# Kernel optimization log

Measured on AMD Instinct MI355X. Metric: run time of the kernel, lower is better.

The kernel has to match this reference:

```python
import jax, jax.numpy as jnp
import numpy as np

D_MODEL = 1024
NUM_HEADS = 16
HEAD_DIM = D_MODEL // NUM_HEADS
B, S = 4, 2048


def setup_inputs() -> dict:
    key = jax.random.key(0)
    ks = jax.random.split(key, 12)
    s = 1.0 / np.sqrt(D_MODEL)
    return {
        "inputs_q": jax.random.normal(ks[0], (B, S, D_MODEL), jnp.float32),
        "inputs_k": jax.random.normal(ks[1], (B, S, D_MODEL), jnp.float32),
        "inputs_v": jax.random.normal(ks[2], (B, S, D_MODEL), jnp.float32),
        "Wq": jax.random.normal(ks[3], (D_MODEL, D_MODEL), jnp.float32) * s,
        "bq": jax.random.normal(ks[4], (D_MODEL,), jnp.float32) * 0.01,
        "Wk": jax.random.normal(ks[5], (D_MODEL, D_MODEL), jnp.float32) * s,
        "bk": jax.random.normal(ks[6], (D_MODEL,), jnp.float32) * 0.01,
        "Wv": jax.random.normal(ks[7], (D_MODEL, D_MODEL), jnp.float32) * s,
        "bv": jax.random.normal(ks[8], (D_MODEL,), jnp.float32) * 0.01,
        "Wo": jax.random.normal(ks[9], (D_MODEL, D_MODEL), jnp.float32) * s,
        "bo": jax.random.normal(ks[10], (D_MODEL,), jnp.float32) * 0.01,
    }


def reference(inputs_q, inputs_k, inputs_v, Wq, bq, Wk, bk, Wv, bv, Wo, bo):
    b, s, _ = inputs_q.shape
    # linear projections
    q = inputs_q @ Wq + bq  # [b, s, d_model]
    k = inputs_k @ Wk + bk
    v = inputs_v @ Wv + bv
    # split heads: bsd -> bhsd
    q = q.reshape(b, s, NUM_HEADS, HEAD_DIM).transpose(0, 2, 1, 3)
    k = k.reshape(b, s, NUM_HEADS, HEAD_DIM).transpose(0, 2, 1, 3)
    v = v.reshape(b, s, NUM_HEADS, HEAD_DIM).transpose(0, 2, 1, 3)
    scale = 1.0 / jnp.sqrt(jnp.asarray(HEAD_DIM, q.dtype))
    scores = jnp.einsum('bhqd,bhkd->bhqk', q, k) * scale  # [b,h,s,s]
    # causal mask: position q attends to k <= q
    causal = jnp.tril(jnp.ones((s, s), dtype=bool))
    scores = jnp.where(causal[None, None], scores, jnp.asarray(-jnp.inf, scores.dtype))
    attn = jax.nn.softmax(scores, axis=-1)
    ctx = jnp.einsum('bhqk,bhkd->bhqd', attn, v)  # [b,h,s,hd]
    ctx = ctx.transpose(0, 2, 1, 3).reshape(b, s, D_MODEL)
    return ctx @ Wo + bo
```

## Files before the change

kernel.cpp:

```cpp
#include <hip/hip_runtime.h>
#include <math.h>
#include <type_traits>

typedef __bf16 bf16;
typedef __attribute__((ext_vector_type(8))) __bf16 bf16x8;
typedef __attribute__((ext_vector_type(4))) float f32x4;

#define SEQ 2048
#define DM 1024
#define NH 16
#define HD 64
#define BATCH 4

#define NEG_BIG (-1e30f)
#define SCALE_L2E 0.18033688011f

__device__ inline bf16x8 cvt_f32x8(const float* p) {
  f32x4 x0 = *(const f32x4*)p;
  f32x4 x1 = *(const f32x4*)(p + 4);
  bf16x8 r;
  r[0] = (bf16)x0[0]; r[1] = (bf16)x0[1]; r[2] = (bf16)x0[2]; r[3] = (bf16)x0[3];
  r[4] = (bf16)x1[0]; r[5] = (bf16)x1[1]; r[6] = (bf16)x1[2]; r[7] = (bf16)x1[3];
  return r;
}

__device__ inline void async_copy16(const bf16* g, bf16* l) {
  __builtin_amdgcn_global_load_lds(
      (const __attribute__((address_space(1))) unsigned int*)g,
      (__attribute__((address_space(3))) unsigned int*)l, 16, 0, 0);
}

__global__ __launch_bounds__(256) void cvt_kernel(const float* __restrict__ src,
                                                  bf16* __restrict__ dst) {
  size_t i = ((size_t)blockIdx.x * 256 + threadIdx.x) * 8;
  *(bf16x8*)(dst + i) = cvt_f32x8(src + i);
}

__global__ __launch_bounds__(256) void transpose_w_kernel(
    const float* __restrict__ Wq, const float* __restrict__ Wk,
    const float* __restrict__ Wv, const float* __restrict__ Wo,
    bf16* __restrict__ Tq, bf16* __restrict__ Tk,
    bf16* __restrict__ Tv, bf16* __restrict__ To) {
  __shared__ bf16 tile[64 * 66];
  int z = blockIdx.z;
  const float* src = (z == 0) ? Wq : (z == 1) ? Wk : (z == 2) ? Wv : Wo;
  bf16* dst = (z == 0) ? Tq : (z == 1) ? Tk : (z == 2) ? Tv : To;
  int n0 = blockIdx.x * 64, k0 = blockIdx.y * 64;
  int t = threadIdx.x;
  int c = t & 63, rr = t >> 6;
#pragma unroll
  for (int i = 0; i < 16; i++) {
    int k = i * 4 + rr;
    tile[k * 66 + c] = (bf16)src[(size_t)(k0 + k) * DM + n0 + c];
  }
  __syncthreads();
#pragma unroll
  for (int i = 0; i < 16; i++) {
    int n = i * 4 + rr;
    dst[(size_t)(n0 + n) * DM + k0 + c] = tile[c * 66 + n];
  }
}

__global__ __launch_bounds__(256) void transpose_v_kernel(
    const bf16* __restrict__ Vc, bf16* __restrict__ Vt) {
  __shared__ bf16 tile[64 * 66];
  int s0 = blockIdx.x * 64;
  int bh = blockIdx.y;
  int t = threadIdx.x;
  int c = t & 63, rr = t >> 6;
  const bf16* src = Vc + (size_t)bh * SEQ * HD;
  bf16* dst = Vt + (size_t)bh * HD * SEQ;
#pragma unroll
  for (int i = 0; i < 16; i++) {
    int s = i * 4 + rr;
    tile[s * 66 + c] = src[(size_t)(s0 + s) * HD + c];
  }
  __syncthreads();
#pragma unroll
  for (int i = 0; i < 16; i++) {
    int d = i * 4 + rr;
    dst[(size_t)d * SEQ + s0 + c] = tile[c * 66 + d];
  }
}

template <typename CT, int MODE>
__global__ __launch_bounds__(256) void gemm_bias_kernel(
    const bf16* __restrict__ A, const bf16* __restrict__ Bt,
    const float* __restrict__ bias, CT* __restrict__ C) {
  __shared__ bf16 As[128 * 32];
  __shared__ bf16 Bs[128 * 32];
  int m0 = blockIdx.x * 128, n0 = blockIdx.y * 128;
  int t = threadIdx.x;
  int wave = t >> 6, lane = t & 63, lr = lane & 15, lq = lane >> 4;
  int wm = (wave & 1) * 64, wn = (wave >> 1) * 64;

  f32x4 acc[4][4];
#pragma unroll
  for (int i = 0; i < 4; i++)
#pragma unroll
    for (int j = 0; j < 4; j++) acc[i][j] = (f32x4){0.f, 0.f, 0.f, 0.f};

  int srow = wave * 32 + (lane >> 2);
  int skc = lane & 3;
  const bf16* gA0 = A + (size_t)(m0 + srow) * DM + skc * 8;
  const bf16* gA1 = gA0 + (size_t)16 * DM;
  const bf16* gB0 = Bt + (size_t)(n0 + srow) * DM + skc * 8;
  const bf16* gB1 = gB0 + (size_t)16 * DM;
  bf16* lA0 = &As[(wave * 128) * 8];
  bf16* lA1 = &As[(wave * 128 + 64) * 8];
  bf16* lB0 = &Bs[(wave * 128) * 8];
  bf16* lB1 = &Bs[(wave * 128 + 64) * 8];

  for (int k0 = 0; k0 < DM; k0 += 32) {
    async_copy16(gA0, lA0);
    async_copy16(gA1, lA1);
    async_copy16(gB0, lB0);
    async_copy16(gB1, lB1);
    gA0 += 32; gA1 += 32; gB0 += 32; gB1 += 32;
    __syncthreads();

    bf16x8 af[4], bfr[4];
#pragma unroll
    for (int i = 0; i < 4; i++)
      af[i] = *(const bf16x8*)&As[(wm + i * 16 + lr) * 32 + lq * 8];
#pragma unroll
    for (int j = 0; j < 4; j++)
      bfr[j] = *(const bf16x8*)&Bs[(wn + j * 16 + lr) * 32 + lq * 8];
#pragma unroll
    for (int i = 0; i < 4; i++)
#pragma unroll
      for (int j = 0; j < 4; j++)
        acc[i][j] = __builtin_amdgcn_mfma_f32_16x16x32_bf16(af[i], bfr[j],
                                                            acc[i][j], 0, 0, 0);
    __syncthreads();
  }

#pragma unroll
  for (int j = 0; j < 4; j++) {
    int col = n0 + wn + j * 16 + lr;
    float bv = bias[col];
#pragma unroll
    for (int i = 0; i < 4; i++) {
      int row0 = m0 + wm + i * 16 + lq * 4;
#pragma unroll
      for (int r = 0; r < 4; r++) {
        int row = row0 + r;
        float v = acc[i][j][r] + bv;
        if constexpr (MODE == 0) {
          C[(size_t)row * DM + col] = (CT)v;
        } else {
          int b = row >> 11, s = row & 2047, h = col >> 6, d = col & 63;
          C[((size_t)(b * NH + h) * SEQ + s) * HD + d] = (CT)v;
        }
      }
    }
  }
}

__global__ __launch_bounds__(256, 2) void attention_kernel(
    const bf16* __restrict__ Qc, const bf16* __restrict__ Kc,
    const bf16* __restrict__ Vt, bf16* __restrict__ ctx) {
  int h = blockIdx.y, b = blockIdx.z;
  int t = threadIdx.x, wave = t >> 6, lane = t & 63, lr = lane & 15,
      lq = lane >> 4;

  int a = blockIdx.x * 2;
  int w4 = (wave + blockIdx.x) & 3;
  int tq = (w4 == 0) ? a : (w4 == 1) ? (63 - a) : (w4 == 2) ? (a + 1) : (62 - a);
  int q0 = tq * 32;

  const bf16* Qb = Qc + (size_t)(b * NH + h) * SEQ * HD;
  const bf16* Kb = Kc + (size_t)(b * NH + h) * SEQ * HD;
  const bf16* Vb = Vt + (size_t)(b * NH + h) * HD * SEQ;
  bf16* Cb = ctx + (size_t)b * SEQ * DM + h * HD;

  bf16x8 qf[2][2];
#pragma unroll
  for (int qi = 0; qi < 2; qi++)
#pragma unroll
    for (int ks = 0; ks < 2; ks++)
      qf[qi][ks] = *(const bf16x8*)&Qb[(size_t)(q0 + qi * 16 + lr) * HD +
                                       ks * 32 + lq * 8];

  f32x4 o[2][4];
  float m_st[2], l_st[2];
#pragma unroll
  for (int mi = 0; mi < 2; mi++) {
#pragma unroll
    for (int dj = 0; dj < 4; dj++) o[mi][dj] = (f32x4){0.f, 0.f, 0.f, 0.f};
    m_st[mi] = NEG_BIG;
    l_st[mi] = 0.f;
  }

  int kv_end = q0 + 32;
#pragma unroll 1
  for (int kv0 = 0; kv0 < kv_end; kv0 += 64) {
    bf16x8 kf[4][2];
#pragma unroll
    for (int kvt = 0; kvt < 4; kvt++)
#pragma unroll
      for (int ks = 0; ks < 2; ks++)
        kf[kvt][ks] = *(const bf16x8*)&Kb[(size_t)(kv0 + kvt * 16 + lr) * HD +
                                          ks * 32 + lq * 8];
    bf16x8 vf[4][2];
#pragma unroll
    for (int dj = 0; dj < 4; dj++)
#pragma unroll
      for (int ks2 = 0; ks2 < 2; ks2++)
        vf[dj][ks2] = *(const bf16x8*)&Vb[(size_t)(dj * 16 + lr) * SEQ + kv0 +
                                          ks2 * 32 + lq * 8];

    f32x4 s[4][2];
#pragma unroll
    for (int kvt = 0; kvt < 4; kvt++)
#pragma unroll
      for (int qi = 0; qi < 2; qi++) {
        f32x4 acc = (f32x4){0.f, 0.f, 0.f, 0.f};
        acc = __builtin_amdgcn_mfma_f32_16x16x32_bf16(kf[kvt][0], qf[qi][0],
                                                      acc, 0, 0, 0);
        acc = __builtin_amdgcn_mfma_f32_16x16x32_bf16(kf[kvt][1], qf[qi][1],
                                                      acc, 0, 0, 0);
        s[kvt][qi] = acc;
      }

    if (kv0 + 63 > q0) {
#pragma unroll
      for (int kvt = 0; kvt < 4; kvt++)
#pragma unroll
        for (int qi = 0; qi < 2; qi++)
#pragma unroll
          for (int r = 0; r < 4; r++) {
            int kv_g = kv0 + kvt * 16 + lq * 4 + r;
            int q_g = q0 + qi * 16 + lr;
            float v = s[kvt][qi][r] * SCALE_L2E;
            s[kvt][qi][r] = (kv_g > q_g) ? NEG_BIG : v;
          }
    } else {
#pragma unroll
      for (int kvt = 0; kvt < 4; kvt++)
#pragma unroll
        for (int qi = 0; qi < 2; qi++)
#pragma unroll
          for (int r = 0; r < 4; r++) s[kvt][qi][r] *= SCALE_L2E;
    }

    float alpha[2];
#pragma unroll
    for (int qi = 0; qi < 2; qi++) {
      float mx = s[0][qi][0];
#pragma unroll
      for (int kvt = 0; kvt < 4; kvt++)
#pragma unroll
        for (int r = 0; r < 4; r++) mx = fmaxf(mx, s[kvt][qi][r]);
      mx = fmaxf(mx, __shfl_xor(mx, 16));
      mx = fmaxf(mx, __shfl_xor(mx, 32));
      float mnew = fmaxf(m_st[qi], mx);
      alpha[qi] = exp2f(m_st[qi] - mnew);
      m_st[qi] = mnew;
      float rs = 0.f;
#pragma unroll
      for (int kvt = 0; kvt < 4; kvt++)
#pragma unroll
        for (int r = 0; r < 4; r++) {
          float pv = exp2f(s[kvt][qi][r] - mnew);
          s[kvt][qi][r] = pv;
          rs += pv;
        }
      rs += __shfl_xor(rs, 16);
      rs += __shfl_xor(rs, 32);
      l_st[qi] = l_st[qi] * alpha[qi] + rs;
    }

    float aT[2][4];
#pragma unroll
    for (int mi = 0; mi < 2; mi++)
#pragma unroll
      for (int r = 0; r < 4; r++) aT[mi][r] = __shfl(alpha[mi], lq * 4 + r);
#pragma unroll
    for (int mi = 0; mi < 2; mi++)
#pragma unroll
      for (int dj = 0; dj < 4; dj++)
#pragma unroll
        for (int r = 0; r < 4; r++) o[mi][dj][r] *= aT[mi][r];

    int src_base = (lq & 1) * 32 + lr;
    bool hi = (lq >> 1) != 0;
#pragma unroll
    for (int ks2 = 0; ks2 < 2; ks2++) {
      unsigned int pk0[2][2], pk1[2][2];
#pragma unroll
      for (int mi = 0; mi < 2; mi++)
#pragma unroll
        for (int w = 0; w < 2; w++) {
          unsigned int r0, r1;
          asm("v_cvt_pk_bf16_f32 %0, %1, %2"
              : "=v"(r0)
              : "v"(s[2 * ks2][mi][2 * w]), "v"(s[2 * ks2][mi][2 * w + 1]));
          asm("v_cvt_pk_bf16_f32 %0, %1, %2"
              : "=v"(r1)
              : "v"(s[2 * ks2 + 1][mi][2 * w]),
                "v"(s[2 * ks2 + 1][mi][2 * w + 1]));
          pk0[mi][w] = r0;
          pk1[mi][w] = r1;
        }
      bf16x8 pf[2];
#pragma unroll
      for (int mi = 0; mi < 2; mi++) {
#pragma unroll
        for (int w = 0; w < 4; w++) {
          int src = src_base + (w >> 1) * 16;
          unsigned int a0 = (unsigned int)__shfl((int)pk0[mi][w & 1], src);
          unsigned int a1 = (unsigned int)__shfl((int)pk1[mi][w & 1], src);
          ((unsigned int*)&pf[mi])[w] = hi ? a1 : a0;
        }
      }
#pragma unroll
      for (int dj = 0; dj < 4; dj++) {
        o[0][dj] = __builtin_amdgcn_mfma_f32_16x16x32_bf16(pf[0], vf[dj][ks2],
                                                           o[0][dj], 0, 0, 0);
        o[1][dj] = __builtin_amdgcn_mfma_f32_16x16x32_bf16(pf[1], vf[dj][ks2],
                                                           o[1][dj], 0, 0, 0);
      }
    }
  }

  float lT[2][4];
#pragma unroll
  for (int mi = 0; mi < 2; mi++)
#pragma unroll
    for (int r = 0; r < 4; r++)
      lT[mi][r] = 1.f / __shfl(l_st[mi], lq * 4 + r);
#pragma unroll
  for (int mi = 0; mi < 2; mi++)
#pragma unroll
    for (int r = 0; r < 4; r++) {
      int row = q0 + mi * 16 + lq * 4 + r;
#pragma unroll
      for (int dj = 0; dj < 4; dj++)
        Cb[(size_t)row * DM + dj * 16 + lr] = (bf16)(o[mi][dj][r] * lT[mi][r]);
    }
}

extern "C" void kernel_launch(void* const* d_in, const int* in_sizes, int n_in,
                              void* d_out, int out_size, void* d_ws,
                              size_t ws_size, hipStream_t stream) {
  const float* iq = (const float*)d_in[0];
  const float* ik = (const float*)d_in[1];
  const float* iv = (const float*)d_in[2];
  const float* Wq = (const float*)d_in[3];
  const float* bq = (const float*)d_in[4];
  const float* Wk = (const float*)d_in[5];
  const float* bk = (const float*)d_in[6];
  const float* Wv = (const float*)d_in[7];
  const float* bv = (const float*)d_in[8];
  const float* Wo = (const float*)d_in[9];
  const float* bo = (const float*)d_in[10];

  char* ws = (char*)d_ws;
  const size_t MB = 1024 * 1024;
  bf16* Tq = (bf16*)(ws + 0 * MB);
  bf16* Tk = (bf16*)(ws + 2 * MB);
  bf16* Tv = (bf16*)(ws + 4 * MB);
  bf16* To = (bf16*)(ws + 6 * MB);
  bf16* Qc = (bf16*)(ws + 8 * MB);
  bf16* Kc = (bf16*)(ws + 24 * MB);
  bf16* Vc = (bf16*)(ws + 40 * MB);
  bf16* X = (bf16*)d_out;
  bf16* Vtp = (bf16*)d_out;
  bf16* Cx = Vc;

  transpose_w_kernel<<<dim3(16, 16, 4), 256, 0, stream>>>(Wq, Wk, Wv, Wo, Tq,
                                                          Tk, Tv, To);
  cvt_kernel<<<dim3(4096), 256, 0, stream>>>(iq, X);
  gemm_bias_kernel<bf16, 1><<<dim3(64, 8), 256, 0, stream>>>(X, Tq, bq, Qc);
  cvt_kernel<<<dim3(4096), 256, 0, stream>>>(ik, X);
  gemm_bias_kernel<bf16, 1><<<dim3(64, 8), 256, 0, stream>>>(X, Tk, bk, Kc);
  cvt_kernel<<<dim3(4096), 256, 0, stream>>>(iv, X);
  gemm_bias_kernel<bf16, 1><<<dim3(64, 8), 256, 0, stream>>>(X, Tv, bv, Vc);
  transpose_v_kernel<<<dim3(32, 64), 256, 0, stream>>>(Vc, Vtp);
  attention_kernel<<<dim3(16, 16, 4), 256, 0, stream>>>(Qc, Kc, Vtp, Cx);
  gemm_bias_kernel<float, 0><<<dim3(64, 8), 256, 0, stream>>>(Cx, To, bo,
                                                              (float*)d_out);
}
```

Measured before the change: 432.3 us.

## Process two adjacent query tiles per wave sharing K/V loads in attention

Each wave now owns two consecutive 32-row query tiles (A and B) and walks the KV sequence in 32-wide steps. Each K/V fragment it loads is reused for both tiles, which roughly halves the global K/V traffic per query row. The grid halves, and wave-to-tile assignment becomes i = blockIdx.x + wv*8 instead of the earlier balanced pairing of front and back tiles. The costs are double the accumulator state per wave, which raises register pressure, smaller KV steps with more softmax rescaling per key, and possibly worse load balance across waves under the causal mask.

```diff
diff --git a/kernel.cpp b/kernel.cpp
--- a/kernel.cpp
+++ b/kernel.cpp
@@ -157,6 +157,145 @@
   }
 }
 
+struct TS {
+  bf16x8 qf[2][2];
+  f32x4 o[2][4];
+  float m_st[2], l_st[2];
+};
+
+__device__ __forceinline__ void proc32(TS& st, const bf16x8 kf[2][2],
+                                       const bf16x8 vf[4], int q0, int kv0,
+                                       bool diag, int lr, int lq) {
+  f32x4 s[2][2];
+#pragma unroll
+  for (int kvt = 0; kvt < 2; kvt++)
+#pragma unroll
+    for (int qi = 0; qi < 2; qi++) {
+      f32x4 acc = (f32x4){0.f, 0.f, 0.f, 0.f};
+      acc = __builtin_amdgcn_mfma_f32_16x16x32_bf16(kf[kvt][0], st.qf[qi][0],
+                                                    acc, 0, 0, 0);
+      acc = __builtin_amdgcn_mfma_f32_16x16x32_bf16(kf[kvt][1], st.qf[qi][1],
+                                                    acc, 0, 0, 0);
+      s[kvt][qi] = acc;
+    }
+
+  if (diag) {
+#pragma unroll
+    for (int kvt = 0; kvt < 2; kvt++)
+#pragma unroll
+      for (int qi = 0; qi < 2; qi++)
+#pragma unroll
+        for (int r = 0; r < 4; r++) {
+          int kv_g = kv0 + kvt * 16 + lq * 4 + r;
+          int q_g = q0 + qi * 16 + lr;
+          float v = s[kvt][qi][r] * SCALE_L2E;
+          s[kvt][qi][r] = (kv_g > q_g) ? NEG_BIG : v;
+        }
+  } else {
+#pragma unroll
+    for (int kvt = 0; kvt < 2; kvt++)
+#pragma unroll
+      for (int qi = 0; qi < 2; qi++)
+#pragma unroll
+        for (int r = 0; r < 4; r++) s[kvt][qi][r] *= SCALE_L2E;
+  }
+
+  float alpha[2];
+#pragma unroll
+  for (int qi = 0; qi < 2; qi++) {
+    float mx = s[0][qi][0];
+#pragma unroll
+    for (int kvt = 0; kvt < 2; kvt++)
+#pragma unroll
+      for (int r = 0; r < 4; r++) mx = fmaxf(mx, s[kvt][qi][r]);
+    mx = fmaxf(mx, __shfl_xor(mx, 16));
+    mx = fmaxf(mx, __shfl_xor(mx, 32));
+    float mnew = fmaxf(st.m_st[qi], mx);
+    alpha[qi] = exp2f(st.m_st[qi] - mnew);
+    st.m_st[qi] = mnew;
+    float rs = 0.f;
+#pragma unroll
+    for (int kvt = 0; kvt < 2; kvt++)
+#pragma unroll
+      for (int r = 0; r < 4; r++) {
+        float pv = exp2f(s[kvt][qi][r] - mnew);
+        s[kvt][qi][r] = pv;
+        rs += pv;
+      }
+    rs += __shfl_xor(rs, 16);
+    rs += __shfl_xor(rs, 32);
+    st.l_st[qi] = st.l_st[qi] * alpha[qi] + rs;
+  }
+
+  float aT[2][4];
+#pragma unroll
+  for (int mi = 0; mi < 2; mi++)
+#pragma unroll
+    for (int r = 0; r < 4; r++) aT[mi][r] = __shfl(alpha[mi], lq * 4 + r);
+#pragma unroll
+  for (int mi = 0; mi < 2; mi++)
+#pragma unroll
+    for (int dj = 0; dj < 4; dj++)
+#pragma unroll
+      for (int r = 0; r < 4; r++) st.o[mi][dj][r] *= aT[mi][r];
+
+  unsigned int pk0[2][2], pk1[2][2];
+#pragma unroll
+  for (int mi = 0; mi < 2; mi++)
+#pragma unroll
+    for (int w = 0; w < 2; w++) {
+      unsigned int r0, r1;
+      asm("v_cvt_pk_bf16_f32 %0, %1, %2"
+          : "=v"(r0)
+          : "v"(s[0][mi][2 * w]), "v"(s[0][mi][2 * w + 1]));
+      asm("v_cvt_pk_bf16_f32 %0, %1, %2"
+          : "=v"(r1)
+          : "v"(s[1][mi][2 * w]), "v"(s[1][mi][2 * w + 1]));
+      pk0[mi][w] = r0;
+      pk1[mi][w] = r1;
+    }
+  int src_base = (lq & 1) * 32 + lr;
+  bool hi = (lq >> 1) != 0;
+  bf16x8 pf[2];
+#pragma unroll
+  for (int mi = 0; mi < 2; mi++) {
+#pragma unroll
+    for (int w = 0; w < 4; w++) {
+      int src = src_base + (w >> 1) * 16;
+      unsigned int a0 = (unsigned int)__shfl((int)pk0[mi][w & 1], src);
+      unsigned int a1 = (unsigned int)__shfl((int)pk1[mi][w & 1], src);
+      ((unsigned int*)&pf[mi])[w] = hi ? a1 : a0;
+    }
+  }
+#pragma unroll
+  for (int dj = 0; dj < 4; dj++) {
+    st.o[0][dj] = __builtin_amdgcn_mfma_f32_16x16x32_bf16(pf[0], vf[dj],
+                                                          st.o[0][dj], 0, 0, 0);
+    st.o[1][dj] = __builtin_amdgcn_mfma_f32_16x16x32_bf16(pf[1], vf[dj],
+                                                          st.o[1][dj], 0, 0, 0);
+  }
+}
+
+__device__ __forceinline__ void epilogue(TS& st, bf16* Cb, int q0, int lr,
+                                         int lq) {
+  float lT[2][4];
+#pragma unroll
+  for (int mi = 0; mi < 2; mi++)
+#pragma unroll
+    for (int r = 0; r < 4; r++)
+      lT[mi][r] = 1.f / __shfl(st.l_st[mi], lq * 4 + r);
+#pragma unroll
+  for (int mi = 0; mi < 2; mi++)
+#pragma unroll
+    for (int r = 0; r < 4; r++) {
+      int row = q0 + mi * 16 + lq * 4 + r;
+#pragma unroll
+      for (int dj = 0; dj < 4; dj++)
+        Cb[(size_t)row * DM + dj * 16 + lr] =
+            (bf16)(st.o[mi][dj][r] * lT[mi][r]);
+    }
+}
+
 __global__ __launch_bounds__(256, 2) void attention_kernel(
     const bf16* __restrict__ Qc, const bf16* __restrict__ Kc,
     const bf16* __restrict__ Vt, bf16* __restrict__ ctx) {
@@ -164,181 +303,75 @@
   int t = threadIdx.x, wave = t >> 6, lane = t & 63, lr = lane & 15,
       lq = lane >> 4;
 
-  int a = blockIdx.x * 2;
-  int w4 = (wave + blockIdx.x) & 3;
-  int tq = (w4 == 0) ? a : (w4 == 1) ? (63 - a) : (w4 == 2) ? (a + 1) : (62 - a);
-  int q0 = tq * 32;
+  int wv = (wave + blockIdx.x) & 3;
+  int i = blockIdx.x + wv * 8;
+  int q0A = (2 * i) * 32;
+  int q0B = q0A + 32;
 
   const bf16* Qb = Qc + (size_t)(b * NH + h) * SEQ * HD;
   const bf16* Kb = Kc + (size_t)(b * NH + h) * SEQ * HD;
   const bf16* Vb = Vt + (size_t)(b * NH + h) * HD * SEQ;
   bf16* Cb = ctx + (size_t)b * SEQ * DM + h * HD;
 
-  bf16x8 qf[2][2];
+  TS A, B;
 #pragma unroll
   for (int qi = 0; qi < 2; qi++)
 #pragma unroll
-    for (int ks = 0; ks < 2; ks++)
-      qf[qi][ks] = *(const bf16x8*)&Qb[(size_t)(q0 + qi * 16 + lr) * HD +
-                                       ks * 32 + lq * 8];
-
-  f32x4 o[2][4];
-  float m_st[2], l_st[2];
+    for (int ks = 0; ks < 2; ks++) {
+      A.qf[qi][ks] = *(const bf16x8*)&Qb[(size_t)(q0A + qi * 16 + lr) * HD +
+                                         ks * 32 + lq * 8];
+      B.qf[qi][ks] = *(const bf16x8*)&Qb[(size_t)(q0B + qi * 16 + lr) * HD +
+                                         ks * 32 + lq * 8];
+    }
 #pragma unroll
   for (int mi = 0; mi < 2; mi++) {
 #pragma unroll
-    for (int dj = 0; dj < 4; dj++) o[mi][dj] = (f32x4){0.f, 0.f, 0.f, 0.f};
-    m_st[mi] = NEG_BIG;
-    l_st[mi] = 0.f;
-  }
-
-  int kv_end = q0 + 32;
+    for (int dj = 0; dj < 4; dj++) {
+      A.o[mi][dj] = (f32x4){0.f, 0.f, 0.f, 0.f};
+      B.o[mi][dj] = (f32x4){0.f, 0.f, 0.f, 0.f};
+    }
+    A.m_st[mi] = NEG_BIG;
+    A.l_st[mi] = 0.f;
+    B.m_st[mi] = NEG_BIG;
+    B.l_st[mi] = 0.f;
+  }
+
+  int endA = q0A + 32;
+  int kv0 = 0;
 #pragma unroll 1
-  for (int kv0 = 0; kv0 < kv_end; kv0 += 64) {
-    bf16x8 kf[4][2];
-#pragma unroll
-    for (int kvt = 0; kvt < 4; kvt++)
+  for (; kv0 < endA; kv0 += 32) {
+    bf16x8 kf[2][2];
+#pragma unroll
+    for (int kvt = 0; kvt < 2; kvt++)
 #pragma unroll
       for (int ks = 0; ks < 2; ks++)
         kf[kvt][ks] = *(const bf16x8*)&Kb[(size_t)(kv0 + kvt * 16 + lr) * HD +
                                           ks * 32 + lq * 8];
-    bf16x8 vf[4][2];
+    bf16x8 vf[4];
 #pragma unroll
     for (int dj = 0; dj < 4; dj++)
-#pragma unroll
-      for (int ks2 = 0; ks2 < 2; ks2++)
-        vf[dj][ks2] = *(const bf16x8*)&Vb[(size_t)(dj * 16 + lr) * SEQ + kv0 +
-                                          ks2 * 32 + lq * 8];
-
-    f32x4 s[4][2];
-#pragma unroll
-    for (int kvt = 0; kvt < 4; kvt++)
-#pragma unroll
-      for (int qi = 0; qi < 2; qi++) {
-        f32x4 acc = (f32x4){0.f, 0.f, 0.f, 0.f};
-        acc = __builtin_amdgcn_mfma_f32_16x16x32_bf16(kf[kvt][0], qf[qi][0],
-                                                      acc, 0, 0, 0);
-        acc = __builtin_amdgcn_mfma_f32_16x16x32_bf16(kf[kvt][1], qf[qi][1],
-                                                      acc, 0, 0, 0);
-        s[kvt][qi] = acc;
-      }
-
-    if (kv0 + 63 > q0) {
-#pragma unroll
-      for (int kvt = 0; kvt < 4; kvt++)
-#pragma unroll
-        for (int qi = 0; qi < 2; qi++)
-#pragma unroll
-          for (int r = 0; r < 4; r++) {
-            int kv_g = kv0 + kvt * 16 + lq * 4 + r;
-            int q_g = q0 + qi * 16 + lr;
-            float v = s[kvt][qi][r] * SCALE_L2E;
-            s[kvt][qi][r] = (kv_g > q_g) ? NEG_BIG : v;
-          }
-    } else {
-#pragma unroll
-      for (int kvt = 0; kvt < 4; kvt++)
-#pragma unroll
-        for (int qi = 0; qi < 2; qi++)
-#pragma unroll
-          for (int r = 0; r < 4; r++) s[kvt][qi][r] *= SCALE_L2E;
-    }
-
-    float alpha[2];
-#pragma unroll
-    for (int qi = 0; qi < 2; qi++) {
-      float mx = s[0][qi][0];
-#pragma unroll
-      for (int kvt = 0; kvt < 4; kvt++)
-#pragma unroll
-        for (int r = 0; r < 4; r++) mx = fmaxf(mx, s[kvt][qi][r]);
-      mx = fmaxf(mx, __shfl_xor(mx, 16));
-      mx = fmaxf(mx, __shfl_xor(mx, 32));
-      float mnew = fmaxf(m_st[qi], mx);
-      alpha[qi] = exp2f(m_st[qi] - mnew);
-      m_st[qi] = mnew;
-      float rs = 0.f;
-#pragma unroll
-      for (int kvt = 0; kvt < 4; kvt++)
-#pragma unroll
-        for (int r = 0; r < 4; r++) {
-          float pv = exp2f(s[kvt][qi][r] - mnew);
-          s[kvt][qi][r] = pv;
-          rs += pv;
-        }
-      rs += __shfl_xor(rs, 16);
-      rs += __shfl_xor(rs, 32);
-      l_st[qi] = l_st[qi] * alpha[qi] + rs;
-    }
-
-    float aT[2][4];
-#pragma unroll
-    for (int mi = 0; mi < 2; mi++)
-#pragma unroll
-      for (int r = 0; r < 4; r++) aT[mi][r] = __shfl(alpha[mi], lq * 4 + r);
-#pragma unroll
-    for (int mi = 0; mi < 2; mi++)
-#pragma unroll
-      for (int dj = 0; dj < 4; dj++)
-#pragma unroll
-        for (int r = 0; r < 4; r++) o[mi][dj][r] *= aT[mi][r];
-
-    int src_base = (lq & 1) * 32 + lr;
-    bool hi = (lq >> 1) != 0;
-#pragma unroll
-    for (int ks2 = 0; ks2 < 2; ks2++) {
-      unsigned int pk0[2][2], pk1[2][2];
-#pragma unroll
-      for (int mi = 0; mi < 2; mi++)
-#pragma unroll
-        for (int w = 0; w < 2; w++) {
-          unsigned int r0, r1;
-          asm("v_cvt_pk_bf16_f32 %0, %1, %2"
-              : "=v"(r0)
-              : "v"(s[2 * ks2][mi][2 * w]), "v"(s[2 * ks2][mi][2 * w + 1]));
-          asm("v_cvt_pk_bf16_f32 %0, %1, %2"
-              : "=v"(r1)
-              : "v"(s[2 * ks2 + 1][mi][2 * w]),
-                "v"(s[2 * ks2 + 1][mi][2 * w + 1]));
-          pk0[mi][w] = r0;
-          pk1[mi][w] = r1;
-        }
-      bf16x8 pf[2];
-#pragma unroll
-      for (int mi = 0; mi < 2; mi++) {
-#pragma unroll
-        for (int w = 0; w < 4; w++) {
-          int src = src_base + (w >> 1) * 16;
-          unsigned int a0 = (unsigned int)__shfl((int)pk0[mi][w & 1], src);
-          unsigned int a1 = (unsigned int)__shfl((int)pk1[mi][w & 1], src);
-          ((unsigned int*)&pf[mi])[w] = hi ? a1 : a0;
-        }
-      }
-#pragma unroll
-      for (int dj = 0; dj < 4; dj++) {
-        o[0][dj] = __builtin_amdgcn_mfma_f32_16x16x32_bf16(pf[0], vf[dj][ks2],
-                                                           o[0][dj], 0, 0, 0);
-        o[1][dj] = __builtin_amdgcn_mfma_f32_16x16x32_bf16(pf[1], vf[dj][ks2],
-                                                           o[1][dj], 0, 0, 0);
-      }
-    }
-  }
-
-  float lT[2][4];
-#pragma unroll
-  for (int mi = 0; mi < 2; mi++)
-#pragma unroll
-    for (int r = 0; r < 4; r++)
-      lT[mi][r] = 1.f / __shfl(l_st[mi], lq * 4 + r);
-#pragma unroll
-  for (int mi = 0; mi < 2; mi++)
-#pragma unroll
-    for (int r = 0; r < 4; r++) {
-      int row = q0 + mi * 16 + lq * 4 + r;
-#pragma unroll
-      for (int dj = 0; dj < 4; dj++)
-        Cb[(size_t)row * DM + dj * 16 + lr] = (bf16)(o[mi][dj][r] * lT[mi][r]);
-    }
+      vf[dj] = *(const bf16x8*)&Vb[(size_t)(dj * 16 + lr) * SEQ + kv0 + lq * 8];
+
+    proc32(A, kf, vf, q0A, kv0, kv0 == q0A, lr, lq);
+    proc32(B, kf, vf, q0B, kv0, false, lr, lq);
+  }
+  {
+    bf16x8 kf[2][2];
+#pragma unroll
+    for (int kvt = 0; kvt < 2; kvt++)
+#pragma unroll
+      for (int ks = 0; ks < 2; ks++)
+        kf[kvt][ks] = *(const bf16x8*)&Kb[(size_t)(kv0 + kvt * 16 + lr) * HD +
+                                          ks * 32 + lq * 8];
+    bf16x8 vf[4];
+#pragma unroll
+    for (int dj = 0; dj < 4; dj++)
+      vf[dj] = *(const bf16x8*)&Vb[(size_t)(dj * 16 + lr) * SEQ + kv0 + lq * 8];
+    proc32(B, kf, vf, q0B, kv0, true, lr, lq);
+  }
+
+  epilogue(A, Cb, q0A, lr, lq);
+  epilogue(B, Cb, q0B, lr, lq);
 }
 
 extern "C" void kernel_launch(void* const* d_in, const int* in_sizes, int n_in,
@@ -378,7 +411,7 @@
   cvt_kernel<<<dim3(4096), 256, 0, stream>>>(iv, X);
   gemm_bias_kernel<bf16, 1><<<dim3(64, 8), 256, 0, stream>>>(X, Tv, bv, Vc);
   transpose_v_kernel<<<dim3(32, 64), 256, 0, stream>>>(Vc, Vtp);
-  attention_kernel<<<dim3(16, 16, 4), 256, 0, stream>>>(Qc, Kc, Vtp, Cx);
+  attention_kernel<<<dim3(8, 16, 4), 256, 0, stream>>>(Qc, Kc, Vtp, Cx);
   gemm_bias_kernel<float, 0><<<dim3(64, 8), 256, 0, stream>>>(Cx, To, bo,
                                                               (float*)d_out);
 }
```

Result: faster. 413.0 us (-4.5%).
